# Kernel optimization log

Hardware: AMD Instinct MI355X
Metric: run time of the kernel (lower is better)

Reference implementation:

```python
import jax, jax.numpy as jnp
import numpy as np

EPS = 1e-5  # InstanceNorm2d default eps


def _branch(emb, Wq, K, Vt, Wo, kv_size):
    # emb: [b,n,c], Wq: [h,c,c] (nn.Linear weight, y = x @ W^T)
    # Qt: [b,h,c,n] = stack_h(emb @ Wq[h]^T).transpose(-1,-2)
    Qt = jnp.einsum('bnc,hdc->bhdn', emb, Wq)
    scores = jnp.einsum('bhdn,bhnk->bhdk', Qt, K) / jnp.sqrt(jnp.float32(kv_size))
    # InstanceNorm2d over heads channel: normalize each [c,kv] map per (b,h), no affine
    m = scores.mean(axis=(-2, -1), keepdims=True)
    v = scores.var(axis=(-2, -1), keepdims=True)
    scores = (scores - m) * jax.lax.rsqrt(v + EPS)
    probs = jax.nn.softmax(scores, axis=-1)            # [b,h,c,kv]
    ctx = jnp.einsum('bhdk,bhkn->bhdn', probs, Vt)     # [b,h,c,n]
    ctx = ctx.mean(axis=1).transpose(0, 2, 1)          # mean over heads -> [b,n,c]
    return ctx @ Wo.T


def setup_inputs() -> dict:
    key = jax.random.key(0)
    ks = jax.random.split(key, 15)
    B, N, H, KV = 16, 196, 4, 960
    C = [64, 128, 256, 512]
    inp = {}
    for i, c in enumerate(C):
        inp[f'emb{i+1}'] = jax.random.normal(ks[i], (B, N, c), jnp.float32)
    inp['emb_all'] = jax.random.normal(ks[4], (B, N, KV), jnp.float32)
    for i, c in enumerate(C):
        inp[f'Wq{i+1}'] = jax.random.normal(ks[5 + i], (H, c, c), jnp.float32) / np.sqrt(c)
    inp['Wk'] = jax.random.normal(ks[9], (H, KV, KV), jnp.float32) / np.sqrt(KV)
    inp['Wv'] = jax.random.normal(ks[10], (H, KV, KV), jnp.float32) / np.sqrt(KV)
    for i, c in enumerate(C):
        inp[f'Wo{i+1}'] = jax.random.normal(ks[11 + i], (c, c), jnp.float32) / np.sqrt(c)
    return inp


def reference(emb1, emb2, emb3, emb4, emb_all,
              Wq1, Wq2, Wq3, Wq4, Wk, Wv, Wo1, Wo2, Wo3, Wo4):
    KV = emb_all.shape[-1]
    # per-head shared K and V: [b,h,n,kv]; Vt = V.transpose(-1,-2): [b,h,kv,n]
    K = jnp.einsum('bnk,hok->bhno', emb_all, Wk)
    Vt = jnp.einsum('bnk,hok->bhon', emb_all, Wv)
    O1 = _branch(emb1, Wq1, K, Vt, Wo1, KV)
    O2 = _branch(emb2, Wq2, K, Vt, Wo2, KV)
    O3 = _branch(emb3, Wq3, K, Vt, Wo3, KV)
    O4 = _branch(emb4, Wq4, K, Vt, Wo4, KV)
    return (O1, O2, O3, O4)
```

## Files before the change

kernel.cpp:

```cpp
#include <hip/hip_runtime.h>
#include <math.h>

#define BB 16
#define NP 196
#define HH 4
#define KVD 960
#define KP 224

typedef __attribute__((ext_vector_type(8))) short s8v;
typedef __attribute__((ext_vector_type(8))) unsigned short u8v;
typedef __attribute__((ext_vector_type(4))) unsigned short u4v;
typedef __attribute__((ext_vector_type(4))) float f4v;

static inline int divup(int a, int b){ return (a+b-1)/b; }
static inline int imin(int a, int b){ return a < b ? a : b; }

__device__ __forceinline__ unsigned short bf16r(float x){
    unsigned int u = __float_as_uint(x);
    u += 0x7fffu + ((u >> 16) & 1u);
    return (unsigned short)(u >> 16);
}
__device__ __forceinline__ float bf16f(unsigned short h){
    return __uint_as_float(((unsigned int)h) << 16);
}

__device__ __forceinline__ void gload16(const unsigned short* g, unsigned short* l){
    __builtin_amdgcn_global_load_lds(
        (const __attribute__((address_space(1))) void*)g,
        (__attribute__((address_space(3))) void*)l, 16, 0, 0);
}

__global__ __launch_bounds__(256)
void decomp_kernel(const float* __restrict__ x, unsigned short* __restrict__ hi,
                   unsigned short* __restrict__ lo, long n4)
{
    for (long i = (long)blockIdx.x * 256 + threadIdx.x; i < n4; i += (long)gridDim.x * 256) {
        float4 v = ((const float4*)x)[i];
        float a[4] = {v.x, v.y, v.z, v.w};
        u4v h, l;
#pragma unroll
        for (int e = 0; e < 4; e++) {
            unsigned short hb = bf16r(a[e]);
            h[e] = hb;
            l[e] = bf16r(a[e] - bf16f(hb));
        }
        *(u4v*)(hi + i * 4) = h;
        *(u4v*)(lo + i * 4) = l;
    }
}

template<int OSPLIT, int STATS>
__global__ __launch_bounds__(256)
void gemm_split(const unsigned short* __restrict__ Ah, const unsigned short* __restrict__ Al,
                const unsigned short* __restrict__ Bh, const unsigned short* __restrict__ Bl,
                float* __restrict__ Cf, unsigned short* __restrict__ Ch,
                unsigned short* __restrict__ Cl, double* __restrict__ part,
                int M, int Nn, int Kk, int ldA, int ldB, int ldC,
                long sAb, long sAh_, long sBb, long sBh_, long sCb, long sCh_,
                int Hdiv, float alpha)
{
    __shared__ u8v AsV[128 * 8];
    __shared__ u8v BsV[128 * 8];
    unsigned short* As = (unsigned short*)AsV;
    unsigned short* Bs = (unsigned short*)BsV;

    int z  = blockIdx.z;
    int bb = z / Hdiv, hz = z - bb * Hdiv;
    const unsigned short* gah = Ah + (long)bb * sAb + (long)hz * sAh_;
    const unsigned short* gal = Al + (long)bb * sAb + (long)hz * sAh_;
    const unsigned short* gbh = Bh + (long)bb * sBb + (long)hz * sBh_;
    const unsigned short* gbl = Bl + (long)bb * sBb + (long)hz * sBh_;
    long coff = (long)bb * sCb + (long)hz * sCh_;

    int t = threadIdx.x;
    int m0 = blockIdx.y * 128, n0 = blockIdx.x * 128;
    int wave = t >> 6, lane = t & 63;
    int wm = wave >> 1, wn = wave & 1;
    int lr = lane & 15, lk = lane >> 4;

    int ls   = (lane & 7) ^ (lane >> 3);
    int comp = ls >> 2;
    int chnk = ls & 3;
    const unsigned short* gA = comp ? gal : gah;
    const unsigned short* gB = comp ? gbl : gbh;
    const unsigned short* aptr[4];
    const unsigned short* bptr[4];
#pragma unroll
    for (int j = 0; j < 4; j++) {
        int ra = m0 + wave * 32 + j * 8 + (lane >> 3);
        ra = (ra < M) ? ra : (M - 1);
        aptr[j] = gA + (long)ra * ldA + chnk * 8;
        int rb = n0 + wave * 32 + j * 8 + (lane >> 3);
        rb = (rb < Nn) ? rb : (Nn - 1);
        bptr[j] = gB + (long)rb * ldB + chnk * 8;
    }

    f4v acc[4][4];
#pragma unroll
    for (int i = 0; i < 4; i++)
#pragma unroll
        for (int j = 0; j < 4; j++) acc[i][j] = (f4v){0.f, 0.f, 0.f, 0.f};

    int nkt = Kk >> 5;
    for (int kt = 0; kt < nkt; ++kt) {
        int k0 = kt << 5;
#pragma unroll
        for (int j = 0; j < 4; j++) {
            gload16(aptr[j] + k0, As + (wave * 4 + j) * 512);
            gload16(bptr[j] + k0, Bs + (wave * 4 + j) * 512);
        }
        __syncthreads();

        s8v afh[4], afl[4], bfh[4], bfl[4];
#pragma unroll
        for (int i = 0; i < 4; i++) {
            int rw = wm * 64 + i * 16 + lr;
            afh[i] = *(const s8v*)&As[rw * 64 + ((lk ^ (rw & 7)) << 3)];
            afl[i] = *(const s8v*)&As[rw * 64 + (((lk + 4) ^ (rw & 7)) << 3)];
            int cw = wn * 64 + i * 16 + lr;
            bfh[i] = *(const s8v*)&Bs[cw * 64 + ((lk ^ (cw & 7)) << 3)];
            bfl[i] = *(const s8v*)&Bs[cw * 64 + (((lk + 4) ^ (cw & 7)) << 3)];
        }
#pragma unroll
        for (int i = 0; i < 4; i++)
#pragma unroll
            for (int j = 0; j < 4; j++) {
                acc[i][j] = __builtin_amdgcn_mfma_f32_16x16x32_bf16(afh[i], bfh[j], acc[i][j], 0, 0, 0);
                acc[i][j] = __builtin_amdgcn_mfma_f32_16x16x32_bf16(afl[i], bfh[j], acc[i][j], 0, 0, 0);
                acc[i][j] = __builtin_amdgcn_mfma_f32_16x16x32_bf16(afh[i], bfl[j], acc[i][j], 0, 0, 0);
            }
        __syncthreads();
    }

    float s1 = 0.f, s2 = 0.f;
#pragma unroll
    for (int i = 0; i < 4; i++)
#pragma unroll
        for (int j = 0; j < 4; j++)
#pragma unroll
            for (int r = 0; r < 4; r++) {
                int gr = m0 + wm * 64 + i * 16 + lk * 4 + r;
                int gc = n0 + wn * 64 + j * 16 + lr;
                if (gr < M) {
                    if (gc < Nn) {
                        float v = acc[i][j][r] * alpha;
                        if (STATS) { s1 += v; s2 += v * v; }
                        if (OSPLIT) {
                            unsigned short hb = bf16r(v);
                            Ch[coff + (long)gr * ldC + gc] = hb;
                            Cl[coff + (long)gr * ldC + gc] = bf16r(v - bf16f(hb));
                        } else {
                            Cf[coff + (long)gr * ldC + gc] = v;
                        }
                    } else if (OSPLIT && gc < ldC) {
                        Ch[coff + (long)gr * ldC + gc] = 0;
                        Cl[coff + (long)gr * ldC + gc] = 0;
                    }
                }
            }

    if (STATS) {
        double* sh = (double*)AsV;
        sh[t] = (double)s1; sh[256 + t] = (double)s2;
        __syncthreads();
        for (int o = 128; o > 0; o >>= 1) {
            if (t < o) { sh[t] += sh[t + o]; sh[256 + t] += sh[256 + t + o]; }
            __syncthreads();
        }
        if (t == 0) {
            atomicAdd(&part[z * 2 + 0], sh[0]);
            atomicAdd(&part[z * 2 + 1], sh[256]);
        }
    }
}

__global__ __launch_bounds__(256)
void pv_fused(const float* __restrict__ Sb, const unsigned short* __restrict__ Vh,
              const unsigned short* __restrict__ Vl, const double* __restrict__ part,
              float* __restrict__ Cb, int c, int m0)
{
    __shared__ unsigned short As[64 * 64];
    __shared__ unsigned short Bs[224 * 64];
    __shared__ float Zlds[64];
    __shared__ float bc2[2];

    int z  = blockIdx.z;
    int gm = m0 + z;
    int bb = gm >> 2, hz = gm & 3;
    int my0 = blockIdx.y * 64;

    int t = threadIdx.x;
    int wave = t >> 6, lane = t & 63;
    int wm = wave >> 1, wn = wave & 1;
    int lr = lane & 15, lk = lane >> 4;

    if (t == 0) {
        double su = part[gm * 2 + 0], sq = part[gm * 2 + 1];
        float inv_e = 1.0f / (float)(c * KVD);
        float mean = (float)(su * (double)inv_e);
        float var  = (float)(sq * (double)inv_e) - mean * mean;
        float is   = rsqrtf(var + 1e-5f);
        bc2[0] = is; bc2[1] = -mean * is;
    }
    __syncthreads();
    float is = bc2[0], dd = bc2[1];

    int arow = t >> 2, achk = t & 3;
    const float* sp = Sb + (size_t)z * c * KVD + (size_t)(my0 + arow) * KVD + achk * 8;
    unsigned short* awh = &As[arow * 64 + (( achk      ^ (arow & 7)) << 3)];
    unsigned short* awl = &As[arow * 64 + (((achk + 4) ^ (arow & 7)) << 3)];

    int ls   = (lane & 7) ^ (lane >> 3);
    int comp = ls >> 2, chnk = ls & 3;
    const unsigned short* vbase = (comp ? Vl : Vh) + (long)bb * (196L * 3840) + hz * 960;
    const unsigned short* bptr[7];
    unsigned short* bdst[7];
#pragma unroll
    for (int q = 0; q < 7; q++) {
        int rlog = (wave * 7 + q) * 8 + (lane >> 3);
        int vrow = (rlog < NP) ? rlog : (NP - 1);
        bptr[q] = vbase + (long)vrow * 3840 + chnk * 8;
        bdst[q] = &Bs[(wave * 7 + q) * 512];
    }

    f4v acc[2][7];
#pragma unroll
    for (int i = 0; i < 2; i++)
#pragma unroll
        for (int j = 0; j < 7; j++) acc[i][j] = (f4v){0.f, 0.f, 0.f, 0.f};
    float zp = 0.f;

    for (int kt = 0; kt < 30; ++kt) {
        int k0 = kt << 5;
#pragma unroll
        for (int q = 0; q < 7; q++) gload16(bptr[q] + k0, bdst[q]);

        float4 v0 = *(const float4*)(sp + k0);
        float4 v1 = *(const float4*)(sp + k0 + 4);
        float s[8] = {v0.x, v0.y, v0.z, v0.w, v1.x, v1.y, v1.z, v1.w};
        u8v hv, lv;
#pragma unroll
        for (int e = 0; e < 8; e++) {
            float p = __expf(fmaf(s[e], is, dd));
            zp += p;
            unsigned short hb = bf16r(p);
            hv[e] = hb;
            lv[e] = bf16r(p - bf16f(hb));
        }
        *(u8v*)awh = hv;
        *(u8v*)awl = lv;
        __syncthreads();

        s8v afh[2], afl[2], bfh[7], bfl[7];
#pragma unroll
        for (int i = 0; i < 2; i++) {
            int ar = wm * 32 + i * 16 + lr;
            afh[i] = *(const s8v*)&As[ar * 64 + ((lk ^ (ar & 7)) << 3)];
            afl[i] = *(const s8v*)&As[ar * 64 + (((lk + 4) ^ (ar & 7)) << 3)];
        }
#pragma unroll
        for (int j = 0; j < 7; j++) {
            int br = wn * 112 + j * 16 + lr;
            bfh[j] = *(const s8v*)&Bs[br * 64 + ((lk ^ (br & 7)) << 3)];
            bfl[j] = *(const s8v*)&Bs[br * 64 + (((lk + 4) ^ (br & 7)) << 3)];
        }
#pragma unroll
        for (int i = 0; i < 2; i++)
#pragma unroll
            for (int j = 0; j < 7; j++) {
                acc[i][j] = __builtin_amdgcn_mfma_f32_16x16x32_bf16(afh[i], bfh[j], acc[i][j], 0, 0, 0);
                acc[i][j] = __builtin_amdgcn_mfma_f32_16x16x32_bf16(afl[i], bfh[j], acc[i][j], 0, 0, 0);
                acc[i][j] = __builtin_amdgcn_mfma_f32_16x16x32_bf16(afh[i], bfl[j], acc[i][j], 0, 0, 0);
            }
        __syncthreads();
    }

    zp += __shfl_xor(zp, 1);
    zp += __shfl_xor(zp, 2);
    if ((t & 3) == 0) Zlds[arow] = zp;
    __syncthreads();

    float rz[2][4];
#pragma unroll
    for (int i = 0; i < 2; i++)
#pragma unroll
        for (int r = 0; r < 4; r++)
            rz[i][r] = 1.0f / Zlds[wm * 32 + i * 16 + lk * 4 + r];

    float* co = Cb + (size_t)gm * c * NP;
#pragma unroll
    for (int i = 0; i < 2; i++)
#pragma unroll
        for (int j = 0; j < 7; j++)
#pragma unroll
            for (int r = 0; r < 4; r++) {
                int grl = wm * 32 + i * 16 + lk * 4 + r;
                int gc  = wn * 112 + j * 16 + lr;
                if (gc < NP)
                    co[(size_t)(my0 + grl) * NP + gc] = acc[i][j][r] * rz[i][r];
            }
}

__global__ __launch_bounds__(256)
void mean_t_kernel(const float* __restrict__ Cb, unsigned short* __restrict__ Mh,
                   unsigned short* __restrict__ Ml, int c)
{
    int b  = blockIdx.z;
    int n0 = blockIdx.x * 32;
    int d0 = blockIdx.y * 32;
    __shared__ float tile[32][33];
    int tx = threadIdx.x & 31;
    int ty = threadIdx.x >> 5;
#pragma unroll
    for (int i = 0; i < 4; i++) {
        int d = d0 + ty + i * 8;
        int n = n0 + tx;
        float s = 0.f;
        if (n < NP) {
#pragma unroll
            for (int h = 0; h < HH; h++)
                s += Cb[(((long)(b * HH + h)) * c + d) * NP + n];
        }
        tile[ty + i * 8][tx] = 0.25f * s;
    }
    __syncthreads();
#pragma unroll
    for (int i = 0; i < 4; i++) {
        int n = n0 + ty + i * 8;
        int d = d0 + tx;
        if (n < NP) {
            float val = tile[tx][ty + i * 8];
            long idx = ((long)b * NP + n) * c + d;
            unsigned short hb = bf16r(val);
            Mh[idx] = hb;
            Ml[idx] = bf16r(val - bf16f(hb));
        }
    }
}

extern "C" void kernel_launch(void* const* d_in, const int* in_sizes, int n_in,
                              void* d_out, int out_size, void* d_ws, size_t ws_size,
                              hipStream_t stream)
{
    const float* embf[4] = {(const float*)d_in[0], (const float*)d_in[1],
                            (const float*)d_in[2], (const float*)d_in[3]};
    const float* emb_all = (const float*)d_in[4];
    const float* Wq[4]   = {(const float*)d_in[5], (const float*)d_in[6],
                            (const float*)d_in[7], (const float*)d_in[8]};
    const float* Wk = (const float*)d_in[9];
    const float* Wv = (const float*)d_in[10];
    const float* Wo[4]   = {(const float*)d_in[11], (const float*)d_in[12],
                            (const float*)d_in[13], (const float*)d_in[14]};
    float* out = (float*)d_out;

    const int Cc[4] = {64, 128, 256, 512};

    char* base = (char*)d_ws;
    size_t off = 0;
    auto carve = [&](size_t bytes) -> void* {
        void* p = base + off;
        off = (off + bytes + 255) & ~(size_t)255;
        return p;
    };

    const long NEA   = (long)BB * NP * KVD;
    const long NWKV  = (long)HH * KVD * KVD;
    const long SUMC2 = 64L*64 + 128L*128 + 256L*256 + 512L*512;

    unsigned short* wkH = (unsigned short*)carve(NWKV * 2);
    unsigned short* wkL = (unsigned short*)carve(NWKV * 2);
    unsigned short* wvH = (unsigned short*)carve(NWKV * 2);
    unsigned short* wvL = (unsigned short*)carve(NWKV * 2);
    unsigned short* wqH = (unsigned short*)carve((long)HH * SUMC2 * 2);
    unsigned short* wqL = (unsigned short*)carve((long)HH * SUMC2 * 2);
    unsigned short* woH = (unsigned short*)carve(SUMC2 * 2);
    unsigned short* woL = (unsigned short*)carve(SUMC2 * 2);
    unsigned short* eaH = (unsigned short*)carve(NEA * 2);
    unsigned short* eaL = (unsigned short*)carve(NEA * 2);
    double* part = (double*)carve(64L * 2 * 8);

    size_t fixed_off = off;
    auto group_bytes = [&](int gb) -> size_t {
        long nbh = (long)gb * HH;
        size_t s = 0;
        auto add = [&](size_t b){ s += (b + 255) & ~(size_t)255; };
        add(nbh * KVD * KP * 2); add(nbh * KVD * KP * 2);
        add((long)gb * NP * HH * KVD * 2); add((long)gb * NP * HH * KVD * 2);
        add(nbh * 512 * KP * 2); add(nbh * 512 * KP * 2);
        add(nbh * 512 * NP * 4);
        add((long)gb * NP * 512 * 2); add((long)gb * NP * 512 * 2);
        add((long)gb * NP * 512 * 2); add((long)gb * NP * 512 * 2);
        return s;
    };
    const size_t minchunk = (size_t)512 * KVD * 4 + (1 << 20);
    int GB = 16;
    while (GB > 1 && fixed_off + group_bytes(GB) + minchunk > ws_size) GB >>= 1;
    const long NBH = (long)GB * HH;

    unsigned short* KtH = (unsigned short*)carve(NBH * KVD * KP * 2);
    unsigned short* KtL = (unsigned short*)carve(NBH * KVD * KP * 2);
    unsigned short* VH  = (unsigned short*)carve((long)GB * NP * HH * KVD * 2);
    unsigned short* VL  = (unsigned short*)carve((long)GB * NP * HH * KVD * 2);
    unsigned short* QtH = (unsigned short*)carve(NBH * 512 * KP * 2);
    unsigned short* QtL = (unsigned short*)carve(NBH * 512 * KP * 2);
    float*  Cb          = (float*)carve(NBH * 512 * NP * 4);
    unsigned short* eiH = (unsigned short*)carve((long)GB * NP * 512 * 2);
    unsigned short* eiL = (unsigned short*)carve((long)GB * NP * 512 * 2);
    unsigned short* MbH = (unsigned short*)carve((long)GB * NP * 512 * 2);
    unsigned short* MbL = (unsigned short*)carve((long)GB * NP * 512 * 2);

    size_t savail = (ws_size > off) ? (ws_size - off) : 0;
    char* chunk = base + off;

    dim3 blk(256);
    const float alphaS = 1.0f / sqrtf((float)KVD);

    auto dec = [&](const float* x, unsigned short* h, unsigned short* l, long n) {
        long n4 = n / 4;
        int g = (int)((n4 + 255) / 256);
        if (g > 1024) g = 1024;
        decomp_kernel<<<g, blk, 0, stream>>>(x, h, l, n4);
    };

    dec(emb_all, eaH, eaL, NEA);
    long wqo[4], woo[4];
    long qo = 0, oo = 0;
    for (int i = 0; i < 4; i++) {
        wqo[i] = qo; dec(Wq[i], wqH + qo, wqL + qo, (long)HH * Cc[i] * Cc[i]);
        qo += (long)HH * Cc[i] * Cc[i];
        woo[i] = oo; dec(Wo[i], woH + oo, woL + oo, (long)Cc[i] * Cc[i]);
        oo += (long)Cc[i] * Cc[i];
    }
    dec(Wk, wkH, wkL, NWKV);
    dec(Wv, wvH, wvL, NWKV);

    long obase[4];
    { long o = 0; for (int i = 0; i < 4; i++) { obase[i] = o; o += (long)BB * NP * Cc[i]; } }

    for (int g0 = 0; g0 < BB; g0 += GB) {
        const unsigned short* eaHg = eaH + (long)g0 * NP * KVD;
        const unsigned short* eaLg = eaL + (long)g0 * NP * KVD;

        gemm_split<1,0><<<dim3(2, 30, GB), blk, 0, stream>>>(
            wkH, wkL, eaHg, eaLg, nullptr, KtH, KtL, nullptr,
            HH * KVD, NP, KVD, KVD, KVD, KP,
            0, 0, (long)NP * KVD, 0,
            (long)HH * KVD * KP, 0, 1, 1.0f);

        gemm_split<1,0><<<dim3(30, 2, GB), blk, 0, stream>>>(
            eaHg, eaLg, wvH, wvL, nullptr, VH, VL, nullptr,
            NP, HH * KVD, KVD, KVD, KVD, HH * KVD,
            (long)NP * KVD, 0, 0, 0,
            (long)NP * HH * KVD, 0, 1, 1.0f);

        for (int i = 0; i < 4; i++) {
            int c = Cc[i];
            dec(embf[i] + (long)g0 * NP * c, eiH, eiL, (long)GB * NP * c);

            gemm_split<1,0><<<dim3(2, divup(HH * c, 128), GB), blk, 0, stream>>>(
                wqH + wqo[i], wqL + wqo[i], eiH, eiL, nullptr, QtH, QtL, nullptr,
                HH * c, NP, c, c, c, KP,
                0, 0, (long)NP * c, 0,
                (long)HH * c * KP, 0, 1, 1.0f);

            hipMemsetAsync(part, 0, 64 * 2 * sizeof(double), stream);

            size_t per = (size_t)c * KVD * 4;
            int G = (savail >= per) ? (int)(savail / per) : 1;
            if (G > (int)NBH) G = (int)NBH;
            if (G < 1) G = 1;
            float* Sb = (float*)chunk;

            for (int m0 = 0; m0 < (int)NBH; m0 += G) {
                int g = imin(G, (int)NBH - m0);
                gemm_split<0,1><<<dim3(8, divup(c, 128), g), blk, 0, stream>>>(
                    QtH + (size_t)m0 * c * KP, QtL + (size_t)m0 * c * KP,
                    KtH + (size_t)m0 * KVD * KP, KtL + (size_t)m0 * KVD * KP,
                    Sb, nullptr, nullptr, part + (size_t)m0 * 2,
                    c, KVD, KP, KP, KP, KVD,
                    (long)c * KP, 0, (long)KVD * KP, 0, (long)c * KVD, 0,
                    1, alphaS);
                pv_fused<<<dim3(1, c / 64, g), blk, 0, stream>>>(
                    Sb, VH, VL, part, Cb, c, m0);
            }
            mean_t_kernel<<<dim3(divup(NP, 32), c / 32, GB), blk, 0, stream>>>(Cb, MbH, MbL, c);
            gemm_split<0,0><<<dim3(divup(c, 128), divup(GB * NP, 128), 1), blk, 0, stream>>>(
                MbH, MbL, woH + woo[i], woL + woo[i],
                out + obase[i] + (long)g0 * NP * c, nullptr, nullptr, nullptr,
                GB * NP, c, c, c, c, c,
                0, 0, 0, 0, 0, 0, 1, 1.0f);
        }
    }
}
```

Baseline: 1.081 ms.

## Batch all bf16 splits into one launch and replace stats atomics with slots

All fifteen fp32-to-bf16 hi/lo splits, including the per-branch embeddings, now run in one launch that takes a segment table, replacing many small launches. The K and V projection GEMMs are re-batched per (batch, head) over z, and V is stored head-major so pv_fused reads contiguous rows. Per-block softmax-normalisation partial sums are written to fixed slots instead of double atomics, which removes the memset per branch. pv_fused then sums those slots serially. The change costs more workspace for the full embedding splits and a bit of serial reduction work.

```diff
diff --git a/kernel.cpp b/kernel.cpp
--- a/kernel.cpp
+++ b/kernel.cpp
@@ -30,10 +30,21 @@
         (__attribute__((address_space(3))) void*)l, 16, 0, 0);
 }
 
+struct DecTable {
+    const float* src[15];
+    unsigned short* dh[15];
+    unsigned short* dl[15];
+    long n4[15];
+};
+
 __global__ __launch_bounds__(256)
-void decomp_kernel(const float* __restrict__ x, unsigned short* __restrict__ hi,
-                   unsigned short* __restrict__ lo, long n4)
+void decomp_all(DecTable T)
 {
+    int seg = blockIdx.y;
+    const float* x = T.src[seg];
+    unsigned short* hi = T.dh[seg];
+    unsigned short* lo = T.dl[seg];
+    long n4 = T.n4[seg];
     for (long i = (long)blockIdx.x * 256 + threadIdx.x; i < n4; i += (long)gridDim.x * 256) {
         float4 v = ((const float4*)x)[i];
         float a[4] = {v.x, v.y, v.z, v.w};
@@ -168,8 +179,9 @@
             __syncthreads();
         }
         if (t == 0) {
-            atomicAdd(&part[z * 2 + 0], sh[0]);
-            atomicAdd(&part[z * 2 + 1], sh[256]);
+            int slot = blockIdx.x + (int)gridDim.x * blockIdx.y;
+            part[(long)z * 64 + slot * 2 + 0] = sh[0];
+            part[(long)z * 64 + slot * 2 + 1] = sh[256];
         }
     }
 }
@@ -177,7 +189,7 @@
 __global__ __launch_bounds__(256)
 void pv_fused(const float* __restrict__ Sb, const unsigned short* __restrict__ Vh,
               const unsigned short* __restrict__ Vl, const double* __restrict__ part,
-              float* __restrict__ Cb, int c, int m0)
+              float* __restrict__ Cb, int c, int m0, int nslot)
 {
     __shared__ unsigned short As[64 * 64];
     __shared__ unsigned short Bs[224 * 64];
@@ -186,7 +198,6 @@
 
     int z  = blockIdx.z;
     int gm = m0 + z;
-    int bb = gm >> 2, hz = gm & 3;
     int my0 = blockIdx.y * 64;
 
     int t = threadIdx.x;
@@ -195,7 +206,9 @@
     int lr = lane & 15, lk = lane >> 4;
 
     if (t == 0) {
-        double su = part[gm * 2 + 0], sq = part[gm * 2 + 1];
+        const double* pp = part + (long)gm * 64;
+        double su = 0.0, sq = 0.0;
+        for (int q = 0; q < nslot; q++) { su += pp[q * 2]; sq += pp[q * 2 + 1]; }
         float inv_e = 1.0f / (float)(c * KVD);
         float mean = (float)(su * (double)inv_e);
         float var  = (float)(sq * (double)inv_e) - mean * mean;
@@ -212,14 +225,14 @@
 
     int ls   = (lane & 7) ^ (lane >> 3);
     int comp = ls >> 2, chnk = ls & 3;
-    const unsigned short* vbase = (comp ? Vl : Vh) + (long)bb * (196L * 3840) + hz * 960;
+    const unsigned short* vbase = (comp ? Vl : Vh) + (long)gm * (196L * KVD);
     const unsigned short* bptr[7];
     unsigned short* bdst[7];
 #pragma unroll
     for (int q = 0; q < 7; q++) {
         int rlog = (wave * 7 + q) * 8 + (lane >> 3);
         int vrow = (rlog < NP) ? rlog : (NP - 1);
-        bptr[q] = vbase + (long)vrow * 3840 + chnk * 8;
+        bptr[q] = vbase + (long)vrow * KVD + chnk * 8;
         bdst[q] = &Bs[(wave * 7 + q) * 512];
     }
 
@@ -377,7 +390,9 @@
     unsigned short* woL = (unsigned short*)carve(SUMC2 * 2);
     unsigned short* eaH = (unsigned short*)carve(NEA * 2);
     unsigned short* eaL = (unsigned short*)carve(NEA * 2);
-    double* part = (double*)carve(64L * 2 * 8);
+    unsigned short* eiH = (unsigned short*)carve(NEA * 2);
+    unsigned short* eiL = (unsigned short*)carve(NEA * 2);
+    double* part = (double*)carve(64L * 64 * 8);
 
     size_t fixed_off = off;
     auto group_bytes = [&](int gb) -> size_t {
@@ -385,10 +400,9 @@
         size_t s = 0;
         auto add = [&](size_t b){ s += (b + 255) & ~(size_t)255; };
         add(nbh * KVD * KP * 2); add(nbh * KVD * KP * 2);
-        add((long)gb * NP * HH * KVD * 2); add((long)gb * NP * HH * KVD * 2);
+        add(nbh * NP * KVD * 2); add(nbh * NP * KVD * 2);
         add(nbh * 512 * KP * 2); add(nbh * 512 * KP * 2);
         add(nbh * 512 * NP * 4);
-        add((long)gb * NP * 512 * 2); add((long)gb * NP * 512 * 2);
         add((long)gb * NP * 512 * 2); add((long)gb * NP * 512 * 2);
         return s;
     };
@@ -399,13 +413,11 @@
 
     unsigned short* KtH = (unsigned short*)carve(NBH * KVD * KP * 2);
     unsigned short* KtL = (unsigned short*)carve(NBH * KVD * KP * 2);
-    unsigned short* VH  = (unsigned short*)carve((long)GB * NP * HH * KVD * 2);
-    unsigned short* VL  = (unsigned short*)carve((long)GB * NP * HH * KVD * 2);
+    unsigned short* VH  = (unsigned short*)carve(NBH * NP * KVD * 2);
+    unsigned short* VL  = (unsigned short*)carve(NBH * NP * KVD * 2);
     unsigned short* QtH = (unsigned short*)carve(NBH * 512 * KP * 2);
     unsigned short* QtL = (unsigned short*)carve(NBH * 512 * KP * 2);
     float*  Cb          = (float*)carve(NBH * 512 * NP * 4);
-    unsigned short* eiH = (unsigned short*)carve((long)GB * NP * 512 * 2);
-    unsigned short* eiL = (unsigned short*)carve((long)GB * NP * 512 * 2);
     unsigned short* MbH = (unsigned short*)carve((long)GB * NP * 512 * 2);
     unsigned short* MbL = (unsigned short*)carve((long)GB * NP * 512 * 2);
 
@@ -415,24 +427,33 @@
     dim3 blk(256);
     const float alphaS = 1.0f / sqrtf((float)KVD);
 
-    auto dec = [&](const float* x, unsigned short* h, unsigned short* l, long n) {
-        long n4 = n / 4;
-        int g = (int)((n4 + 255) / 256);
-        if (g > 1024) g = 1024;
-        decomp_kernel<<<g, blk, 0, stream>>>(x, h, l, n4);
-    };
-
-    dec(emb_all, eaH, eaL, NEA);
-    long wqo[4], woo[4];
-    long qo = 0, oo = 0;
-    for (int i = 0; i < 4; i++) {
-        wqo[i] = qo; dec(Wq[i], wqH + qo, wqL + qo, (long)HH * Cc[i] * Cc[i]);
-        qo += (long)HH * Cc[i] * Cc[i];
-        woo[i] = oo; dec(Wo[i], woH + oo, woL + oo, (long)Cc[i] * Cc[i]);
-        oo += (long)Cc[i] * Cc[i];
-    }
-    dec(Wk, wkH, wkL, NWKV);
-    dec(Wv, wvH, wvL, NWKV);
+    long eio[4], wqo[4], woo[4];
+    { long eo = 0, qo = 0, oo = 0;
+      for (int i = 0; i < 4; i++) {
+          eio[i] = eo; eo += (long)BB * NP * Cc[i];
+          wqo[i] = qo; qo += (long)HH * Cc[i] * Cc[i];
+          woo[i] = oo; oo += (long)Cc[i] * Cc[i];
+      } }
+    {
+        DecTable T;
+        int k = 0;
+        for (int i = 0; i < 4; i++) {
+            T.src[k] = embf[i]; T.dh[k] = eiH + eio[i]; T.dl[k] = eiL + eio[i];
+            T.n4[k] = ((long)BB * NP * Cc[i]) / 4; k++;
+        }
+        T.src[k] = emb_all; T.dh[k] = eaH; T.dl[k] = eaL; T.n4[k] = NEA / 4; k++;
+        for (int i = 0; i < 4; i++) {
+            T.src[k] = Wq[i]; T.dh[k] = wqH + wqo[i]; T.dl[k] = wqL + wqo[i];
+            T.n4[k] = ((long)HH * Cc[i] * Cc[i]) / 4; k++;
+        }
+        T.src[k] = Wk; T.dh[k] = wkH; T.dl[k] = wkL; T.n4[k] = NWKV / 4; k++;
+        T.src[k] = Wv; T.dh[k] = wvH; T.dl[k] = wvL; T.n4[k] = NWKV / 4; k++;
+        for (int i = 0; i < 4; i++) {
+            T.src[k] = Wo[i]; T.dh[k] = woH + woo[i]; T.dl[k] = woL + woo[i];
+            T.n4[k] = ((long)Cc[i] * Cc[i]) / 4; k++;
+        }
+        decomp_all<<<dim3(512, 15, 1), blk, 0, stream>>>(T);
+    }
 
     long obase[4];
     { long o = 0; for (int i = 0; i < 4; i++) { obase[i] = o; o += (long)BB * NP * Cc[i]; } }
@@ -441,29 +462,30 @@
         const unsigned short* eaHg = eaH + (long)g0 * NP * KVD;
         const unsigned short* eaLg = eaL + (long)g0 * NP * KVD;
 
-        gemm_split<1,0><<<dim3(2, 30, GB), blk, 0, stream>>>(
+        gemm_split<1,0><<<dim3(2, 8, (int)NBH), blk, 0, stream>>>(
             wkH, wkL, eaHg, eaLg, nullptr, KtH, KtL, nullptr,
-            HH * KVD, NP, KVD, KVD, KVD, KP,
-            0, 0, (long)NP * KVD, 0,
-            (long)HH * KVD * KP, 0, 1, 1.0f);
-
-        gemm_split<1,0><<<dim3(30, 2, GB), blk, 0, stream>>>(
+            KVD, NP, KVD, KVD, KVD, KP,
+            0, (long)KVD * KVD, (long)NP * KVD, 0,
+            (long)HH * KVD * KP, (long)KVD * KP, HH, 1.0f);
+
+        gemm_split<1,0><<<dim3(8, 2, (int)NBH), blk, 0, stream>>>(
             eaHg, eaLg, wvH, wvL, nullptr, VH, VL, nullptr,
-            NP, HH * KVD, KVD, KVD, KVD, HH * KVD,
-            (long)NP * KVD, 0, 0, 0,
-            (long)NP * HH * KVD, 0, 1, 1.0f);
+            NP, KVD, KVD, KVD, KVD, KVD,
+            (long)NP * KVD, 0, 0, (long)KVD * KVD,
+            (long)HH * NP * KVD, (long)NP * KVD, HH, 1.0f);
 
         for (int i = 0; i < 4; i++) {
             int c = Cc[i];
-            dec(embf[i] + (long)g0 * NP * c, eiH, eiL, (long)GB * NP * c);
 
             gemm_split<1,0><<<dim3(2, divup(HH * c, 128), GB), blk, 0, stream>>>(
-                wqH + wqo[i], wqL + wqo[i], eiH, eiL, nullptr, QtH, QtL, nullptr,
+                wqH + wqo[i], wqL + wqo[i],
+                eiH + eio[i] + (long)g0 * NP * c, eiL + eio[i] + (long)g0 * NP * c,
+                nullptr, QtH, QtL, nullptr,
                 HH * c, NP, c, c, c, KP,
                 0, 0, (long)NP * c, 0,
                 (long)HH * c * KP, 0, 1, 1.0f);
 
-            hipMemsetAsync(part, 0, 64 * 2 * sizeof(double), stream);
+            int nslot = 8 * divup(c, 128);
 
             size_t per = (size_t)c * KVD * 4;
             int G = (savail >= per) ? (int)(savail / per) : 1;
@@ -476,12 +498,12 @@
                 gemm_split<0,1><<<dim3(8, divup(c, 128), g), blk, 0, stream>>>(
                     QtH + (size_t)m0 * c * KP, QtL + (size_t)m0 * c * KP,
                     KtH + (size_t)m0 * KVD * KP, KtL + (size_t)m0 * KVD * KP,
-                    Sb, nullptr, nullptr, part + (size_t)m0 * 2,
+                    Sb, nullptr, nullptr, part + (size_t)m0 * 64,
                     c, KVD, KP, KP, KP, KVD,
                     (long)c * KP, 0, (long)KVD * KP, 0, (long)c * KVD, 0,
                     1, alphaS);
                 pv_fused<<<dim3(1, c / 64, g), blk, 0, stream>>>(
-                    Sb, VH, VL, part, Cb, c, m0);
+                    Sb, VH, VL, part, Cb, c, m0, nslot);
             }
             mean_t_kernel<<<dim3(divup(NP, 32), c / 32, GB), blk, 0, stream>>>(Cb, MbH, MbL, c);
             gemm_split<0,0><<<dim3(divup(c, 128), divup(GB * NP, 128), 1), blk, 0, stream>>>(
```

Result: slower. 1.113 ms (+2.9%).
